# Performance work log

Hardware: AMD Instinct MI355X
Metric: run time of the kernel (lower is better)

The kernel has to match this reference:

```python
import jax, jax.numpy as jnp
import numpy as np

N, E, IN_DIM, HID = 100000, 1600000, 128, 64


def setup_inputs() -> dict:
    key = jax.random.key(0)
    ks = jax.random.split(key, 10)
    inv = lambda f: 1.0 / np.sqrt(f)
    return {
        "x": jax.random.normal(ks[0], (N, IN_DIM), jnp.float32),
        "edge_index": jax.random.randint(ks[1], (2, E), 0, N, dtype=jnp.int32),
        "fc_w": jax.random.normal(ks[2], (IN_DIM, HID), jnp.float32) * inv(IN_DIM),
        "fc_b": jnp.zeros((HID,), jnp.float32),
        "conv1_w": jax.random.normal(ks[3], (HID, HID), jnp.float32) * inv(HID),
        "conv1_b": jnp.zeros((HID,), jnp.float32),
        "conv2_w": jax.random.normal(ks[4], (HID, HID), jnp.float32) * inv(HID),
        "conv2_b": jnp.zeros((HID,), jnp.float32),
        "node_w": jax.random.normal(ks[5], (HID, 1), jnp.float32) * inv(HID),
        "node_b": jnp.zeros((1,), jnp.float32),
        "edge_w": jax.random.normal(ks[6], (2 * HID, 1), jnp.float32) * inv(2 * HID),
        "edge_b": jnp.zeros((1,), jnp.float32),
    }


def _gcn_norm(row, col):
    # PyG GCNConv default: add self-loops, symmetric D^-1/2 (A+I) D^-1/2 norm.
    loops = jnp.arange(N, dtype=row.dtype)
    rows = jnp.concatenate([row, loops])
    cols = jnp.concatenate([col, loops])
    deg = jax.ops.segment_sum(jnp.ones(rows.shape[0], jnp.float32), cols, num_segments=N)
    dinv = jax.lax.rsqrt(jnp.maximum(deg, 1.0))  # deg >= 1 due to self-loops
    norm = dinv[rows] * dinv[cols]  # [E+N]
    return rows, cols, norm


def _gcn_conv(h, rows, cols, norm, W, b):
    m = h @ W                                   # [N, HID] transform first (out==in dim)
    agg = jax.ops.segment_sum(m[rows] * norm[:, None], cols, num_segments=N)
    return agg + b


def reference(x, edge_index, fc_w, fc_b, conv1_w, conv1_b, conv2_w, conv2_b,
              node_w, node_b, edge_w, edge_b):
    # Dropout layers act as identity in eval mode.
    row, col = edge_index[0], edge_index[1]
    rows, cols, norm = _gcn_norm(row, col)

    h = x @ fc_w + fc_b                          # [N, HID]
    h = jax.nn.relu(_gcn_conv(h, rows, cols, norm, conv1_w, conv1_b))
    h = jax.nn.relu(_gcn_conv(h, rows, cols, norm, conv2_w, conv2_b))

    node_score = jax.nn.sigmoid(h @ node_w + node_b)  # [N, 1]

    # edge_score = sigmoid(cat([h[row], h[col]]) @ edge_w + b)
    # == sigmoid(h[row] @ edge_w[:HID] + h[col] @ edge_w[HID:] + b)
    s_src = h @ edge_w[:HID]                     # [N, 1]
    s_dst = h @ edge_w[HID:]                     # [N, 1]
    edge_score = jax.nn.sigmoid(s_src[row] + s_dst[col] + edge_b)  # [E, 1]
    return edge_score, node_score
```

## Files before the change

kernel.cpp:

```cpp
#include <hip/hip_runtime.h>
#include <math.h>

constexpr int NN  = 100000;
constexpr int EE  = 1600000;
constexpr int IND = 128;
constexpr int HID = 64;

constexpr int NBUCK = (NN + 127) / 128;
constexpr int CAP   = 2432;
constexpr int CHUNK = 4096;
constexpr int NTILE = NN / 16;

using bf16x8 = __attribute__((ext_vector_type(8))) short;
using f32x4v = __attribute__((ext_vector_type(4))) float;

__device__ __forceinline__ unsigned short f2bf(float f) {
    union { float f; unsigned int u; } v; v.f = f;
    unsigned int r = (v.u + 0x7FFFu + ((v.u >> 16) & 1u)) >> 16;
    return (unsigned short)r;
}
__device__ __forceinline__ void unp(unsigned int u, float& lo, float& hi) {
    union { unsigned int x; float f; } a, c;
    a.x = u << 16; c.x = u & 0xFFFF0000u;
    lo = a.f; hi = c.f;
}

#define ACC4(u) do { float l_, h_; \
    unp((u).x, l_, h_); a0 += l_; a1 += h_; \
    unp((u).y, l_, h_); a2 += l_; a3 += h_; } while (0)


__global__ __launch_bounds__(256) void k_zero(int* __restrict__ p, int n) {
    int i = blockIdx.x * 256 + threadIdx.x;
    if (i < n) p[i] = 0;
}


__global__ __launch_bounds__(256) void k_bscatter(const int* __restrict__ row, const int* __restrict__ col,
                                                  int* __restrict__ gcur, int* __restrict__ ebuf) {
    __shared__ int lhist[NBUCK];
    __shared__ int lbase[NBUCK];
    __shared__ int lcur[NBUCK];
    const int tx = threadIdx.x;
    const int cbase = blockIdx.x * CHUNK;

    for (int b = tx; b < NBUCK; b += 256) lhist[b] = 0;
    __syncthreads();

    #pragma unroll
    for (int i = 0; i < CHUNK / 256; ++i) {
        int e = cbase + tx + i * 256;
        if (e < EE) atomicAdd(&lhist[col[e] >> 7], 1);
    }
    __syncthreads();

    for (int b = tx; b < NBUCK; b += 256) {
        int c = lhist[b];
        if (c) lbase[b] = atomicAdd(&gcur[b], c);
        lcur[b] = 0;
    }
    __syncthreads();

    #pragma unroll
    for (int i = 0; i < CHUNK / 256; ++i) {
        int e = cbase + tx + i * 256;
        if (e < EE) {
            int c = col[e];
            int b = c >> 7;
            int rank = atomicAdd(&lcur[b], 1);
            ebuf[b * CAP + lbase[b] + rank] = (row[e] << 7) | (c & 127);
        }
    }
}


__global__ __launch_bounds__(256) void k_bsortip(const int* __restrict__ gcur, int* __restrict__ ebuf,
                                                 int* __restrict__ bc, float* __restrict__ dinv) {
    __shared__ int ebl[CAP];
    __shared__ int h[128];
    __shared__ int sc[128];
    __shared__ int cur[128];
    const int tx = threadIdx.x;
    const int b = blockIdx.x;
    const int cnt = gcur[b];
    int* eb = ebuf + b * CAP;

    if (tx < 128) h[tx] = 0;
    for (int e = tx; e < cnt; e += 256) ebl[e] = eb[e];
    __syncthreads();
    for (int e = tx; e < cnt; e += 256) atomicAdd(&h[ebl[e] & 127], 1);
    __syncthreads();

    if (tx < 128) sc[tx] = h[tx];
    __syncthreads();
    #pragma unroll
    for (int o = 1; o < 128; o <<= 1) {
        int add = (tx < 128 && tx >= o) ? sc[tx - o] : 0;
        __syncthreads();
        if (tx < 128) sc[tx] += add;
        __syncthreads();
    }
    if (tx < 128) {
        int ex = sc[tx] - h[tx];
        cur[tx] = ex;
        int g = b * 128 + tx;
        if (g < NN) {
            bc[g]   = (ex << 16) | h[tx];
            dinv[g] = rsqrtf((float)(h[tx] + 1));
        }
    }
    __syncthreads();

    for (int e = tx; e < cnt; e += 256) {
        int v = ebl[e];
        int r = atomicAdd(&cur[v & 127], 1);
        eb[r] = v >> 7;
    }
}


__global__ __launch_bounds__(256) void k_wc(const float* __restrict__ wfc, const float* __restrict__ bfc,
                                            const float* __restrict__ w1, const float* __restrict__ w2,
                                            unsigned short* __restrict__ wct, float* __restrict__ bvec,
                                            unsigned short* __restrict__ w2t) {
    int b = blockIdx.x, tx = threadIdx.x;
    if (b < 32) {
        int idx = b * 256 + tx;
        int k = idx >> 6, c = idx & 63;
        float acc = 0.f;
        #pragma unroll 8
        for (int j = 0; j < 64; ++j) acc += wfc[k * HID + j] * w1[j * HID + c];
        wct[c * IND + k] = f2bf(acc);
    } else if (b < 48) {
        int idx = (b - 32) * 256 + tx;
        int k = idx >> 6, c = idx & 63;
        w2t[c * HID + k] = f2bf(w2[k * HID + c]);
    } else if (tx < 64) {
        float acc = 0.f;
        #pragma unroll 8
        for (int j = 0; j < 64; ++j) acc += bfc[j] * w1[j * HID + tx];
        bvec[tx] = acc;
    }
}


__global__ __launch_bounds__(256) void k_mmx(const float* __restrict__ x,
        const unsigned short* __restrict__ wct, const float* __restrict__ bvec,
        const float* __restrict__ dinv, unsigned short* __restrict__ mdb) {
    const int tx = threadIdx.x;
    const int lane = tx & 63;
    const int wv = tx >> 6;
    const int l15 = lane & 15, g = lane >> 4;
    const int tile = blockIdx.x * 4 + wv;
    if (tile >= NTILE) return;
    const int row0 = tile * 16;

    bf16x8 bf[4][4];
    #pragma unroll
    for (int t = 0; t < 4; ++t) {
        const unsigned short* bp = wct + (t * 16 + l15) * IND + g * 8;
        #pragma unroll
        for (int kc = 0; kc < 4; ++kc)
            bf[t][kc] = *(const bf16x8*)(bp + kc * 32);
    }

    const float* ap = x + (row0 + l15) * IND + g * 8;
    bf16x8 af[4];
    #pragma unroll
    for (int kc = 0; kc < 4; ++kc) {
        float4 lo = *(const float4*)(ap + kc * 32);
        float4 hi = *(const float4*)(ap + kc * 32 + 4);
        bf16x8 f;
        f[0] = (short)f2bf(lo.x); f[1] = (short)f2bf(lo.y);
        f[2] = (short)f2bf(lo.z); f[3] = (short)f2bf(lo.w);
        f[4] = (short)f2bf(hi.x); f[5] = (short)f2bf(hi.y);
        f[6] = (short)f2bf(hi.z); f[7] = (short)f2bf(hi.w);
        af[kc] = f;
    }

    f32x4v acc[4];
    #pragma unroll
    for (int t = 0; t < 4; ++t) {
        float bv = bvec[t * 16 + l15];
        acc[t][0] = bv; acc[t][1] = bv; acc[t][2] = bv; acc[t][3] = bv;
    }
    #pragma unroll
    for (int kc = 0; kc < 4; ++kc) {
        #pragma unroll
        for (int t = 0; t < 4; ++t)
            acc[t] = __builtin_amdgcn_mfma_f32_16x16x32_bf16(af[kc], bf[t][kc], acc[t], 0, 0, 0);
    }

    #pragma unroll
    for (int r = 0; r < 4; ++r) {
        int rowg = row0 + g * 4 + r;
        float di = dinv[rowg];
        #pragma unroll
        for (int t = 0; t < 4; ++t)
            mdb[rowg * HID + t * 16 + l15] = f2bf(acc[t][r] * di);
    }
}


__global__ __launch_bounds__(256) void k_mm2x(const unsigned short* __restrict__ h1b,
        const unsigned short* __restrict__ w2t, const float* __restrict__ dinv,
        unsigned short* __restrict__ mdb) {
    const int tx = threadIdx.x;
    const int lane = tx & 63;
    const int wv = tx >> 6;
    const int l15 = lane & 15, g = lane >> 4;
    const int tile = blockIdx.x * 4 + wv;
    if (tile >= NTILE) return;
    const int row0 = tile * 16;

    bf16x8 bf[4][2];
    #pragma unroll
    for (int t = 0; t < 4; ++t) {
        const unsigned short* bp = w2t + (t * 16 + l15) * HID + g * 8;
        #pragma unroll
        for (int kc = 0; kc < 2; ++kc)
            bf[t][kc] = *(const bf16x8*)(bp + kc * 32);
    }

    const unsigned short* ap = h1b + (row0 + l15) * HID + g * 8;
    bf16x8 af[2];
    af[0] = *(const bf16x8*)(ap);
    af[1] = *(const bf16x8*)(ap + 32);

    f32x4v acc[4] = {};
    #pragma unroll
    for (int kc = 0; kc < 2; ++kc) {
        #pragma unroll
        for (int t = 0; t < 4; ++t)
            acc[t] = __builtin_amdgcn_mfma_f32_16x16x32_bf16(af[kc], bf[t][kc], acc[t], 0, 0, 0);
    }

    #pragma unroll
    for (int r = 0; r < 4; ++r) {
        int rowg = row0 + g * 4 + r;
        float di = dinv[rowg];
        #pragma unroll
        for (int t = 0; t < 4; ++t)
            mdb[rowg * HID + t * 16 + l15] = f2bf(acc[t][r] * di);
    }
}


__global__ __launch_bounds__(256) void k_gather(const unsigned short* __restrict__ mdb,
                                                const int* __restrict__ prow, const int* __restrict__ bc,
                                                const float* __restrict__ dinv, const float* __restrict__ b,
                                                unsigned short* __restrict__ hout) {
    const uint2* mdq = (const uint2*)mdb;
    int lane = threadIdx.x & 63;
    int q    = lane >> 4;
    int f4   = lane & 15;
    int wid  = (blockIdx.x * blockDim.x + threadIdx.x) >> 6;
    int nwv  = (gridDim.x * blockDim.x) >> 6;
    float4 bj = *(const float4*)&b[f4 * 4];

    for (int i = wid; i < NN; i += nwv) {
        int vv = bc[i];
        int s = (i >> 7) * CAP + (vv >> 16);
        int n = vv & 0xFFFF;
        float a0 = 0.f, a1 = 0.f, a2 = 0.f, a3 = 0.f;
        if (q == 0) {
            uint2 u = mdq[i * 16 + f4];
            ACC4(u);
        }
        for (int e = 0; e < n; e += 16) {
            int e0 = e + q, e1 = e + 4 + q, e2 = e + 8 + q, e3 = e + 12 + q;
            int r0 = prow[s + (e0 < n ? e0 : 0)];
            int r1 = prow[s + (e1 < n ? e1 : 0)];
            int r2 = prow[s + (e2 < n ? e2 : 0)];
            int r3 = prow[s + (e3 < n ? e3 : 0)];
            uint2 u0 = mdq[r0 * 16 + f4];
            uint2 u1 = mdq[r1 * 16 + f4];
            uint2 u2 = mdq[r2 * 16 + f4];
            uint2 u3 = mdq[r3 * 16 + f4];
            if (e1 >= n) { u1.x = 0u; u1.y = 0u; }
            if (e2 >= n) { u2.x = 0u; u2.y = 0u; }
            if (e3 >= n) { u3.x = 0u; u3.y = 0u; }
            if (e0 >= n) { u0.x = 0u; u0.y = 0u; }
            ACC4(u0); ACC4(u1); ACC4(u2); ACC4(u3);
        }
        a0 += __shfl_xor(a0, 32, 64); a1 += __shfl_xor(a1, 32, 64);
        a2 += __shfl_xor(a2, 32, 64); a3 += __shfl_xor(a3, 32, 64);
        a0 += __shfl_xor(a0, 16, 64); a1 += __shfl_xor(a1, 16, 64);
        a2 += __shfl_xor(a2, 16, 64); a3 += __shfl_xor(a3, 16, 64);

        float di = dinv[i];
        if (q == 0) {
            ushort4 o;
            o.x = f2bf(fmaxf(di * a0 + bj.x, 0.f));
            o.y = f2bf(fmaxf(di * a1 + bj.y, 0.f));
            o.z = f2bf(fmaxf(di * a2 + bj.z, 0.f));
            o.w = f2bf(fmaxf(di * a3 + bj.w, 0.f));
            *(ushort4*)&hout[i * HID + f4 * 4] = o;
        }
    }
}


__global__ __launch_bounds__(256) void k_gather2s(const unsigned short* __restrict__ mdb,
        const int* __restrict__ prow, const int* __restrict__ bc, const float* __restrict__ dinv,
        const float* __restrict__ b, const float* __restrict__ nw, const float* __restrict__ nb,
        const float* __restrict__ ew, float* __restrict__ out_node,
        float* __restrict__ ssrc, float* __restrict__ sdst) {
    const uint2* mdq = (const uint2*)mdb;
    int lane = threadIdx.x & 63;
    int q    = lane >> 4;
    int f4   = lane & 15;
    int wid  = (blockIdx.x * blockDim.x + threadIdx.x) >> 6;
    int nwv  = (gridDim.x * blockDim.x) >> 6;
    float4 bj  = *(const float4*)&b[f4 * 4];
    float4 wn  = *(const float4*)&nw[f4 * 4];
    float4 we1 = *(const float4*)&ew[f4 * 4];
    float4 we2 = *(const float4*)&ew[64 + f4 * 4];
    float nb0 = nb[0];

    for (int i = wid; i < NN; i += nwv) {
        int vv = bc[i];
        int s = (i >> 7) * CAP + (vv >> 16);
        int n = vv & 0xFFFF;
        float a0 = 0.f, a1 = 0.f, a2 = 0.f, a3 = 0.f;
        if (q == 0) {
            uint2 u = mdq[i * 16 + f4];
            ACC4(u);
        }
        for (int e = 0; e < n; e += 16) {
            int e0 = e + q, e1 = e + 4 + q, e2 = e + 8 + q, e3 = e + 12 + q;
            int r0 = prow[s + (e0 < n ? e0 : 0)];
            int r1 = prow[s + (e1 < n ? e1 : 0)];
            int r2 = prow[s + (e2 < n ? e2 : 0)];
            int r3 = prow[s + (e3 < n ? e3 : 0)];
            uint2 u0 = mdq[r0 * 16 + f4];
            uint2 u1 = mdq[r1 * 16 + f4];
            uint2 u2 = mdq[r2 * 16 + f4];
            uint2 u3 = mdq[r3 * 16 + f4];
            if (e1 >= n) { u1.x = 0u; u1.y = 0u; }
            if (e2 >= n) { u2.x = 0u; u2.y = 0u; }
            if (e3 >= n) { u3.x = 0u; u3.y = 0u; }
            if (e0 >= n) { u0.x = 0u; u0.y = 0u; }
            ACC4(u0); ACC4(u1); ACC4(u2); ACC4(u3);
        }
        a0 += __shfl_xor(a0, 32, 64); a1 += __shfl_xor(a1, 32, 64);
        a2 += __shfl_xor(a2, 32, 64); a3 += __shfl_xor(a3, 32, 64);
        a0 += __shfl_xor(a0, 16, 64); a1 += __shfl_xor(a1, 16, 64);
        a2 += __shfl_xor(a2, 16, 64); a3 += __shfl_xor(a3, 16, 64);

        float di = dinv[i];
        float v0 = fmaxf(di * a0 + bj.x, 0.f);
        float v1 = fmaxf(di * a1 + bj.y, 0.f);
        float v2 = fmaxf(di * a2 + bj.z, 0.f);
        float v3 = fmaxf(di * a3 + bj.w, 0.f);

        float a  = v0 * wn.x  + v1 * wn.y  + v2 * wn.z  + v3 * wn.w;
        float s1 = v0 * we1.x + v1 * we1.y + v2 * we1.z + v3 * we1.w;
        float s2 = v0 * we2.x + v1 * we2.y + v2 * we2.z + v3 * we2.w;
        #pragma unroll
        for (int off = 8; off; off >>= 1) {
            a  += __shfl_xor(a,  off, 64);
            s1 += __shfl_xor(s1, off, 64);
            s2 += __shfl_xor(s2, off, 64);
        }
        if (lane == 0) {
            out_node[i] = 1.f / (1.f + expf(-(a + nb0)));
            ssrc[i] = s1;
            sdst[i] = s2;
        }
    }
}


__global__ __launch_bounds__(256) void k_edge(const int4* __restrict__ row4, const int4* __restrict__ col4,
                                              const float* __restrict__ ssrc, const float* __restrict__ sdst,
                                              const float* __restrict__ eb, float4* __restrict__ out4) {
    constexpr int NQ = EE / 4;
    int i = blockIdx.x * 256 + threadIdx.x;
    if (i >= NQ) return;
    float eb0 = eb[0];
    int4 r = row4[i], c = col4[i];
    float4 o;
    float z;
    z = ssrc[r.x] + sdst[c.x] + eb0; o.x = 1.f / (1.f + expf(-z));
    z = ssrc[r.y] + sdst[c.y] + eb0; o.y = 1.f / (1.f + expf(-z));
    z = ssrc[r.z] + sdst[c.z] + eb0; o.z = 1.f / (1.f + expf(-z));
    z = ssrc[r.w] + sdst[c.w] + eb0; o.w = 1.f / (1.f + expf(-z));
    out4[i] = o;
}

extern "C" void kernel_launch(void* const* d_in, const int* in_sizes, int n_in,
                              void* d_out, int out_size, void* d_ws, size_t ws_size,
                              hipStream_t stream) {
    const float* x    = (const float*)d_in[0];
    const int*   ei   = (const int*)d_in[1];
    const float* fc_w = (const float*)d_in[2];
    const float* fc_b = (const float*)d_in[3];
    const float* c1w  = (const float*)d_in[4];
    const float* c1b  = (const float*)d_in[5];
    const float* c2w  = (const float*)d_in[6];
    const float* c2b  = (const float*)d_in[7];
    const float* nw   = (const float*)d_in[8];
    const float* nb   = (const float*)d_in[9];
    const float* ew   = (const float*)d_in[10];
    const float* eb   = (const float*)d_in[11];
    const int* row = ei;
    const int* col = ei + EE;

    constexpr int NP = 100352;
    float* ws   = (float*)d_ws;
    float* dinv = ws;
    int*   bc   = (int*)(ws + NP);
    int*   gcur = (int*)(ws + 2 * NP);
    unsigned short* wct = (unsigned short*)(ws + 2 * NP + 1024);
    float* bvec = ws + 2 * NP + 1024 + 4096;
    unsigned short* w2t = (unsigned short*)(bvec + 128);
    int*   ebuf = (int*)(bvec + 128 + 2048);
    float* Areg = (float*)(ebuf + NBUCK * CAP);
    unsigned short* h1b = (unsigned short*)Areg;
    unsigned short* Bbf = (unsigned short*)(Areg + (size_t)NN * HID / 2);
    float* ssrc = Areg;
    float* sdst = Areg + NP;

    float* out_edge = (float*)d_out;
    float* out_node = out_edge + EE;

    const int nbC = (EE + CHUNK - 1) / CHUNK;
    const int nbQ = (EE / 4 + 255) / 256;
    const int nbM = (NTILE + 3) / 4;

    k_zero    <<<(NBUCK + 255) / 256, 256, 0, stream>>>(gcur, NBUCK);
    k_bscatter<<<nbC, 256, 0, stream>>>(row, col, gcur, ebuf);
    k_bsortip <<<NBUCK, 256, 0, stream>>>(gcur, ebuf, bc, dinv);

    k_wc    <<<49, 256, 0, stream>>>(fc_w, fc_b, c1w, c2w, wct, bvec, w2t);
    k_mmx   <<<nbM, 256, 0, stream>>>(x, wct, bvec, dinv, Bbf);
    k_gather<<<2048, 256, 0, stream>>>(Bbf, ebuf, bc, dinv, c1b, h1b);

    k_mm2x    <<<nbM, 256, 0, stream>>>(h1b, w2t, dinv, Bbf);
    k_gather2s<<<2048, 256, 0, stream>>>(Bbf, ebuf, bc, dinv, c2b,
                                         nw, nb, ew, out_node, ssrc, sdst);

    k_edge<<<nbQ, 256, 0, stream>>>((const int4*)row, (const int4*)col,
                                    ssrc, sdst, eb, (float4*)out_edge);
}
```

Baseline: 187.2 us.

## Fold self-loops into CSR, pre-scale indices, merge weight prep into scatter

```diff
diff --git a/kernel.cpp b/kernel.cpp
--- a/kernel.cpp
+++ b/kernel.cpp
@@ -7,9 +7,10 @@
 constexpr int HID = 64;
 
 constexpr int NBUCK = (NN + 127) / 128;
-constexpr int CAP   = 2432;
+constexpr int CAP   = 2560;
 constexpr int CHUNK = 4096;
 constexpr int NTILE = NN / 16;
+constexpr int NCB   = (EE + CHUNK - 1) / CHUNK;
 
 using bf16x8 = __attribute__((ext_vector_type(8))) short;
 using f32x4v = __attribute__((ext_vector_type(4))) float;
@@ -37,11 +38,39 @@
 
 
 __global__ __launch_bounds__(256) void k_bscatter(const int* __restrict__ row, const int* __restrict__ col,
-                                                  int* __restrict__ gcur, int* __restrict__ ebuf) {
+                                                  int* __restrict__ gcur, int* __restrict__ ebuf,
+                                                  const float* __restrict__ wfc, const float* __restrict__ bfc,
+                                                  const float* __restrict__ w1, const float* __restrict__ w2,
+                                                  unsigned short* __restrict__ wct, float* __restrict__ bvec,
+                                                  unsigned short* __restrict__ w2t) {
     __shared__ int lhist[NBUCK];
     __shared__ int lbase[NBUCK];
     __shared__ int lcur[NBUCK];
+    __shared__ int lcol[CHUNK];
     const int tx = threadIdx.x;
+
+    if (blockIdx.x >= NCB) {
+        int b = blockIdx.x - NCB;
+        if (b < 32) {
+            int idx = b * 256 + tx;
+            int k = idx >> 6, c = idx & 63;
+            float acc = 0.f;
+            #pragma unroll 8
+            for (int j = 0; j < 64; ++j) acc += wfc[k * HID + j] * w1[j * HID + c];
+            wct[c * IND + k] = f2bf(acc);
+        } else if (b < 48) {
+            int idx = (b - 32) * 256 + tx;
+            int k = idx >> 6, c = idx & 63;
+            w2t[c * HID + k] = f2bf(w2[k * HID + c]);
+        } else if (tx < 64) {
+            float acc = 0.f;
+            #pragma unroll 8
+            for (int j = 0; j < 64; ++j) acc += bfc[j] * w1[j * HID + tx];
+            bvec[tx] = acc;
+        }
+        return;
+    }
+
     const int cbase = blockIdx.x * CHUNK;
 
     for (int b = tx; b < NBUCK; b += 256) lhist[b] = 0;
@@ -50,7 +79,9 @@
     #pragma unroll
     for (int i = 0; i < CHUNK / 256; ++i) {
         int e = cbase + tx + i * 256;
-        if (e < EE) atomicAdd(&lhist[col[e] >> 7], 1);
+        int c = (e < EE) ? col[e] : -1;
+        lcol[tx + i * 256] = c;
+        if (c >= 0) atomicAdd(&lhist[c >> 7], 1);
     }
     __syncthreads();
 
@@ -65,7 +96,7 @@
     for (int i = 0; i < CHUNK / 256; ++i) {
         int e = cbase + tx + i * 256;
         if (e < EE) {
-            int c = col[e];
+            int c = lcol[tx + i * 256];
             int b = c >> 7;
             int rank = atomicAdd(&lcur[b], 1);
             ebuf[b * CAP + lbase[b] + rank] = (row[e] << 7) | (c & 127);
@@ -91,7 +122,7 @@
     for (int e = tx; e < cnt; e += 256) atomicAdd(&h[ebl[e] & 127], 1);
     __syncthreads();
 
-    if (tx < 128) sc[tx] = h[tx];
+    if (tx < 128) sc[tx] = h[tx] + 1;
     __syncthreads();
     #pragma unroll
     for (int o = 1; o < 128; o <<= 1) {
@@ -101,12 +132,14 @@
         __syncthreads();
     }
     if (tx < 128) {
-        int ex = sc[tx] - h[tx];
-        cur[tx] = ex;
+        int n1 = h[tx] + 1;
+        int ex = sc[tx] - n1;
+        cur[tx] = ex + 1;
         int g = b * 128 + tx;
+        eb[ex] = g << 7;
         if (g < NN) {
-            bc[g]   = (ex << 16) | h[tx];
-            dinv[g] = rsqrtf((float)(h[tx] + 1));
+            bc[g]   = (ex << 16) | n1;
+            dinv[g] = rsqrtf((float)n1);
         }
     }
     __syncthreads();
@@ -114,32 +147,7 @@
     for (int e = tx; e < cnt; e += 256) {
         int v = ebl[e];
         int r = atomicAdd(&cur[v & 127], 1);
-        eb[r] = v >> 7;
-    }
-}
-
-
-__global__ __launch_bounds__(256) void k_wc(const float* __restrict__ wfc, const float* __restrict__ bfc,
-                                            const float* __restrict__ w1, const float* __restrict__ w2,
-                                            unsigned short* __restrict__ wct, float* __restrict__ bvec,
-                                            unsigned short* __restrict__ w2t) {
-    int b = blockIdx.x, tx = threadIdx.x;
-    if (b < 32) {
-        int idx = b * 256 + tx;
-        int k = idx >> 6, c = idx & 63;
-        float acc = 0.f;
-        #pragma unroll 8
-        for (int j = 0; j < 64; ++j) acc += wfc[k * HID + j] * w1[j * HID + c];
-        wct[c * IND + k] = f2bf(acc);
-    } else if (b < 48) {
-        int idx = (b - 32) * 256 + tx;
-        int k = idx >> 6, c = idx & 63;
-        w2t[c * HID + k] = f2bf(w2[k * HID + c]);
-    } else if (tx < 64) {
-        float acc = 0.f;
-        #pragma unroll 8
-        for (int j = 0; j < 64; ++j) acc += bfc[j] * w1[j * HID + tx];
-        bvec[tx] = acc;
+        eb[r] = v & 0xFFFFFF80;
     }
 }
 
@@ -247,40 +255,36 @@
 
 
 __global__ __launch_bounds__(256) void k_gather(const unsigned short* __restrict__ mdb,
-                                                const int* __restrict__ prow, const int* __restrict__ bc,
+                                                const int* __restrict__ ebuf, const int* __restrict__ bc,
                                                 const float* __restrict__ dinv, const float* __restrict__ b,
                                                 unsigned short* __restrict__ hout) {
-    const uint2* mdq = (const uint2*)mdb;
     int lane = threadIdx.x & 63;
     int q    = lane >> 4;
     int f4   = lane & 15;
     int wid  = (blockIdx.x * blockDim.x + threadIdx.x) >> 6;
     int nwv  = (gridDim.x * blockDim.x) >> 6;
     float4 bj = *(const float4*)&b[f4 * 4];
+    const char* mbase = (const char*)mdb + f4 * 8;
 
     for (int i = wid; i < NN; i += nwv) {
         int vv = bc[i];
-        int s = (i >> 7) * CAP + (vv >> 16);
+        const int* pr = ebuf + (i >> 7) * CAP + (vv >> 16);
         int n = vv & 0xFFFF;
         float a0 = 0.f, a1 = 0.f, a2 = 0.f, a3 = 0.f;
-        if (q == 0) {
-            uint2 u = mdq[i * 16 + f4];
-            ACC4(u);
-        }
         for (int e = 0; e < n; e += 16) {
             int e0 = e + q, e1 = e + 4 + q, e2 = e + 8 + q, e3 = e + 12 + q;
-            int r0 = prow[s + (e0 < n ? e0 : 0)];
-            int r1 = prow[s + (e1 < n ? e1 : 0)];
-            int r2 = prow[s + (e2 < n ? e2 : 0)];
-            int r3 = prow[s + (e3 < n ? e3 : 0)];
-            uint2 u0 = mdq[r0 * 16 + f4];
-            uint2 u1 = mdq[r1 * 16 + f4];
-            uint2 u2 = mdq[r2 * 16 + f4];
-            uint2 u3 = mdq[r3 * 16 + f4];
+            int r0 = pr[e0 < n ? e0 : 0];
+            int r1 = pr[e1 < n ? e1 : 0];
+            int r2 = pr[e2 < n ? e2 : 0];
+            int r3 = pr[e3 < n ? e3 : 0];
+            uint2 u0 = *(const uint2*)(mbase + r0);
+            uint2 u1 = *(const uint2*)(mbase + r1);
+            uint2 u2 = *(const uint2*)(mbase + r2);
+            uint2 u3 = *(const uint2*)(mbase + r3);
+            if (e0 >= n) { u0.x = 0u; u0.y = 0u; }
             if (e1 >= n) { u1.x = 0u; u1.y = 0u; }
             if (e2 >= n) { u2.x = 0u; u2.y = 0u; }
             if (e3 >= n) { u3.x = 0u; u3.y = 0u; }
-            if (e0 >= n) { u0.x = 0u; u0.y = 0u; }
             ACC4(u0); ACC4(u1); ACC4(u2); ACC4(u3);
         }
         a0 += __shfl_xor(a0, 32, 64); a1 += __shfl_xor(a1, 32, 64);
@@ -288,8 +292,8 @@
         a0 += __shfl_xor(a0, 16, 64); a1 += __shfl_xor(a1, 16, 64);
         a2 += __shfl_xor(a2, 16, 64); a3 += __shfl_xor(a3, 16, 64);
 
-        float di = dinv[i];
         if (q == 0) {
+            float di = dinv[i];
             ushort4 o;
             o.x = f2bf(fmaxf(di * a0 + bj.x, 0.f));
             o.y = f2bf(fmaxf(di * a1 + bj.y, 0.f));
@@ -302,11 +306,10 @@
 
 
 __global__ __launch_bounds__(256) void k_gather2s(const unsigned short* __restrict__ mdb,
-        const int* __restrict__ prow, const int* __restrict__ bc, const float* __restrict__ dinv,
+        const int* __restrict__ ebuf, const int* __restrict__ bc, const float* __restrict__ dinv,
         const float* __restrict__ b, const float* __restrict__ nw, const float* __restrict__ nb,
         const float* __restrict__ ew, float* __restrict__ out_node,
         float* __restrict__ ssrc, float* __restrict__ sdst) {
-    const uint2* mdq = (const uint2*)mdb;
     int lane = threadIdx.x & 63;
     int q    = lane >> 4;
     int f4   = lane & 15;
@@ -317,30 +320,27 @@
     float4 we1 = *(const float4*)&ew[f4 * 4];
     float4 we2 = *(const float4*)&ew[64 + f4 * 4];
     float nb0 = nb[0];
+    const char* mbase = (const char*)mdb + f4 * 8;
 
     for (int i = wid; i < NN; i += nwv) {
         int vv = bc[i];
-        int s = (i >> 7) * CAP + (vv >> 16);
+        const int* pr = ebuf + (i >> 7) * CAP + (vv >> 16);
         int n = vv & 0xFFFF;
         float a0 = 0.f, a1 = 0.f, a2 = 0.f, a3 = 0.f;
-        if (q == 0) {
-            uint2 u = mdq[i * 16 + f4];
-            ACC4(u);
-        }
         for (int e = 0; e < n; e += 16) {
             int e0 = e + q, e1 = e + 4 + q, e2 = e + 8 + q, e3 = e + 12 + q;
-            int r0 = prow[s + (e0 < n ? e0 : 0)];
-            int r1 = prow[s + (e1 < n ? e1 : 0)];
-            int r2 = prow[s + (e2 < n ? e2 : 0)];
-            int r3 = prow[s + (e3 < n ? e3 : 0)];
-            uint2 u0 = mdq[r0 * 16 + f4];
-            uint2 u1 = mdq[r1 * 16 + f4];
-            uint2 u2 = mdq[r2 * 16 + f4];
-            uint2 u3 = mdq[r3 * 16 + f4];
+            int r0 = pr[e0 < n ? e0 : 0];
+            int r1 = pr[e1 < n ? e1 : 0];
+            int r2 = pr[e2 < n ? e2 : 0];
+            int r3 = pr[e3 < n ? e3 : 0];
+            uint2 u0 = *(const uint2*)(mbase + r0);
+            uint2 u1 = *(const uint2*)(mbase + r1);
+            uint2 u2 = *(const uint2*)(mbase + r2);
+            uint2 u3 = *(const uint2*)(mbase + r3);
+            if (e0 >= n) { u0.x = 0u; u0.y = 0u; }
             if (e1 >= n) { u1.x = 0u; u1.y = 0u; }
             if (e2 >= n) { u2.x = 0u; u2.y = 0u; }
             if (e3 >= n) { u3.x = 0u; u3.y = 0u; }
-            if (e0 >= n) { u0.x = 0u; u0.y = 0u; }
             ACC4(u0); ACC4(u1); ACC4(u2); ACC4(u3);
         }
         a0 += __shfl_xor(a0, 32, 64); a1 += __shfl_xor(a1, 32, 64);
@@ -425,15 +425,14 @@
     float* out_edge = (float*)d_out;
     float* out_node = out_edge + EE;
 
-    const int nbC = (EE + CHUNK - 1) / CHUNK;
     const int nbQ = (EE / 4 + 255) / 256;
     const int nbM = (NTILE + 3) / 4;
 
     k_zero    <<<(NBUCK + 255) / 256, 256, 0, stream>>>(gcur, NBUCK);
-    k_bscatter<<<nbC, 256, 0, stream>>>(row, col, gcur, ebuf);
+    k_bscatter<<<NCB + 49, 256, 0, stream>>>(row, col, gcur, ebuf,
+                                             fc_w, fc_b, c1w, c2w, wct, bvec, w2t);
     k_bsortip <<<NBUCK, 256, 0, stream>>>(gcur, ebuf, bc, dinv);
 
-    k_wc    <<<49, 256, 0, stream>>>(fc_w, fc_b, c1w, c2w, wct, bvec, w2t);
     k_mmx   <<<nbM, 256, 0, stream>>>(x, wct, bvec, dinv, Bbf);
     k_gather<<<2048, 256, 0, stream>>>(Bbf, ebuf, bc, dinv, c1b, h1b);
 
```

Result: faster. 178.5 us (-4.7%).
